# Performance work log

Hardware: AMD Instinct MI355X
Metric: run time of the kernel (lower is better)

Reference implementation:

```python
import jax, jax.numpy as jnp
import numpy as np

N = 100000      # nodes
E = 1600000     # edges (avg degree 16)
D = 64          # in_channels == conv widths == lin width
G = 64          # graphs in batch
OUT = 10        # out_channels


def setup_inputs() -> dict:
    key = jax.random.key(0)
    ks = jax.random.split(key, 20)
    s = 0.1
    inp = {
        "x": jax.random.normal(ks[0], (N, D), jnp.float32),
        "edge_index": jax.random.randint(ks[1], (2, E), 0, N, dtype=jnp.int64),
        "batch": jnp.sort(jax.random.randint(ks[2], (N,), 0, G, dtype=jnp.int64)),
    }
    k = 3
    for i in range(3):  # 3 SAGEConv layers: lin_l (Wl, bl) on aggregated, lin_r (Wr, no bias) on root
        inp[f"c{i}_Wl"] = jax.random.normal(ks[k], (D, D), jnp.float32) * s; k += 1
        inp[f"c{i}_bl"] = jnp.zeros((D,), jnp.float32)
        inp[f"c{i}_Wr"] = jax.random.normal(ks[k], (D, D), jnp.float32) * s; k += 1
    inp["l0_W"] = jax.random.normal(ks[k], (D, D), jnp.float32) * s; k += 1
    inp["l0_b"] = jnp.zeros((D,), jnp.float32)
    inp["out_W"] = jax.random.normal(ks[k], (D, OUT), jnp.float32) * s; k += 1
    inp["out_b"] = jnp.zeros((OUT,), jnp.float32)
    return inp


def reference(x, edge_index, batch,
              c0_Wl, c0_bl, c0_Wr,
              c1_Wl, c1_bl, c1_Wr,
              c2_Wl, c2_bl, c2_Wr,
              l0_W, l0_b, out_W, out_b):
    src, dst = edge_index[0], edge_index[1]
    # in-degree of each target node (mean conv aggregation), computed once
    deg = jax.ops.segment_sum(jnp.ones((E,), x.dtype), dst, num_segments=N)
    inv_deg = (1.0 / jnp.maximum(deg, 1.0))[:, None]

    def sage(h, Wl, bl, Wr):
        # gather source features, mean-aggregate at targets, then lin_l(agg) + lin_r(h)
        agg = jax.ops.segment_sum(h[src], dst, num_segments=N) * inv_deg
        return agg @ Wl + bl + h @ Wr

    h = jax.nn.relu(sage(x, c0_Wl, c0_bl, c0_Wr))
    h = jax.nn.relu(sage(h, c1_Wl, c1_bl, c1_Wr))
    h = jax.nn.relu(sage(h, c2_Wl, c2_bl, c2_Wr))

    # global mean pool over graphs
    cnt = jax.ops.segment_sum(jnp.ones((N,), h.dtype), batch, num_segments=G)
    g = jax.ops.segment_sum(h, batch, num_segments=G) / jnp.maximum(cnt, 1.0)[:, None]

    g = jax.nn.relu(g @ l0_W + l0_b)
    return g @ out_W + out_b  # [G, OUT]
```

## Files before the change

kernel.cpp:

```cpp
#include <hip/hip_runtime.h>
#include <hip/hip_fp16.h>

#define WPB 8
#define PADK 136
#define BSH 8
#define BNODES 256
#define SC_BLOCKS 256
#define HIST_BLOCKS 256
#define HSTRIDE 512

typedef _Float16 half8 __attribute__((ext_vector_type(8)));
typedef _Float16 half2v __attribute__((ext_vector_type(2)));
typedef float floatx4 __attribute__((ext_vector_type(4)));
typedef float floatx2 __attribute__((ext_vector_type(2)));

__global__ __launch_bounds__(256) void gnn_pre(const int* __restrict__ dst,
                                               int* __restrict__ bkt_cnt, int nbkt, int E,
                                               const int* __restrict__ batch,
                                               float* __restrict__ gcnt, int N,
                                               const float4* __restrict__ xin,
                                               ushort4* __restrict__ x16o, int n4,
                                               __half* __restrict__ x16,
                                               __half* __restrict__ hA,
                                               __half* __restrict__ hB,
                                               int* __restrict__ hist_all) {
    int tid = threadIdx.x;
    if (blockIdx.x < HIST_BLOCKS) {
        __shared__ int h[512];
        __shared__ int gb[64];
        for (int i = tid; i < nbkt; i += 256) h[i] = 0;
        if (tid < 64) gb[tid] = 0;
        __syncthreads();
        const int stride = HIST_BLOCKS * 256;
        for (int e = blockIdx.x * 256 + tid; e < E; e += stride)
            atomicAdd(&h[dst[e] >> BSH], 1);
        for (int i = blockIdx.x * 256 + tid; i < N; i += stride)
            atomicAdd(&gb[batch[i]], 1);
        __syncthreads();
        for (int i = tid; i < nbkt; i += 256) {
            int v = h[i];
            hist_all[blockIdx.x * HSTRIDE + i] = v;
            if (v) atomicAdd(&bkt_cnt[i], v);
        }
        if (tid < 64) {
            int v = gb[tid];
            if (v) atomicAdd(&gcnt[tid], (float)v);
        }
        if (blockIdx.x == 0 && tid < 64) {
            x16[(size_t)N * 64 + tid] = __ushort_as_half((unsigned short)0);
            hA[(size_t)N * 64 + tid] = __ushort_as_half((unsigned short)0);
            hB[(size_t)N * 64 + tid] = __ushort_as_half((unsigned short)0);
        }
    } else {
        int i = (blockIdx.x - HIST_BLOCKS) * 256 + tid;
        if (i < n4) {
            float4 f = xin[i];
            ushort4 o;
            o.x = __half_as_ushort(__float2half(f.x));
            o.y = __half_as_ushort(__float2half(f.y));
            o.z = __half_as_ushort(__float2half(f.z));
            o.w = __half_as_ushort(__float2half(f.w));
            x16o[i] = o;
        }
    }
}

__global__ void gnn_bkt_scan(const int* __restrict__ bkt_cnt, int* __restrict__ bkt_base,
                             int* __restrict__ row_ptr, int nbkt, int N) {
    int lane = threadIdx.x;
    int carry = 0;
    for (int base = 0; base < nbkt; base += 64) {
        int idx = base + lane;
        int v = (idx < nbkt) ? bkt_cnt[idx] : 0;
        int x = v;
#pragma unroll
        for (int off = 1; off < 64; off <<= 1) {
            int y = __shfl_up(x, off);
            if (lane >= off) x += y;
        }
        if (idx < nbkt) bkt_base[idx] = carry + (x - v);
        carry += __shfl(x, 63);
    }
    if (lane == 0) {
        bkt_base[nbkt] = carry;
        row_ptr[N] = carry;
    }
}

__global__ __launch_bounds__(256) void gnn_scan2(const int* __restrict__ hist_all,
                                                 const int* __restrict__ bkt_base,
                                                 int* __restrict__ blk_base_all, int nbkt) {
    int b = blockIdx.x;
    int t = threadIdx.x, lane = t & 63, wv = t >> 6;
    __shared__ int wsum[4];
    int v = hist_all[t * HSTRIDE + b];
    int x = v;
#pragma unroll
    for (int off = 1; off < 64; off <<= 1) {
        int y = __shfl_up(x, off);
        if (lane >= off) x += y;
    }
    if (lane == 63) wsum[wv] = x;
    __syncthreads();
    int wexcl = 0;
    for (int w = 0; w < wv; w++) wexcl += wsum[w];
    blk_base_all[t * HSTRIDE + b] = bkt_base[b] + wexcl + (x - v);
}

__global__ __launch_bounds__(256) void gnn_bkt_scatter(const int* __restrict__ src,
                                                       const int* __restrict__ dst,
                                                       const int* __restrict__ blk_base_all,
                                                       unsigned int* __restrict__ pairs,
                                                       int E, int nbkt) {
    __shared__ int cur[512];
    int tid = threadIdx.x;
    for (int i = tid; i < nbkt; i += 256) cur[i] = blk_base_all[blockIdx.x * HSTRIDE + i];
    __syncthreads();
    const int stride = SC_BLOCKS * 256;
    for (int e = blockIdx.x * 256 + tid; e < E; e += stride) {
        int d = dst[e];
        int b = d >> BSH;
        int p = atomicAdd(&cur[b], 1);
        pairs[p] = (unsigned int)src[e] | ((unsigned int)(d & (BNODES - 1)) << 24);
    }
}

__global__ __launch_bounds__(256) void gnn_bkt_csr(const unsigned int* __restrict__ pairs,
                                                   const int* __restrict__ bkt_base,
                                                   int* __restrict__ row_ptr,
                                                   float* __restrict__ inv_deg,
                                                   int* __restrict__ csr_src, int N) {
    __shared__ int hist[BNODES];
    __shared__ int excl[BNODES];
    __shared__ int cur[BNODES];
    int b = blockIdx.x;
    int base = bkt_base[b];
    int cnt = bkt_base[b + 1] - base;
    int nd0 = b << BSH;
    int tid = threadIdx.x;
    hist[tid] = 0;
    __syncthreads();
    for (int i = tid; i < cnt; i += 256) atomicAdd(&hist[pairs[base + i] >> 24], 1);
    __syncthreads();
    if (tid < 64) {
        int carry = 0;
#pragma unroll
        for (int c = 0; c < BNODES; c += 64) {
            int v = hist[c + tid];
            int x = v;
#pragma unroll
            for (int off = 1; off < 64; off <<= 1) {
                int y = __shfl_up(x, off);
                if (tid >= off) x += y;
            }
            excl[c + tid] = carry + (x - v);
            carry += __shfl(x, 63);
        }
    }
    __syncthreads();
    {
        int node = nd0 + tid;
        if (node < N) {
            row_ptr[node] = base + excl[tid];
            int d = hist[tid];
            inv_deg[node] = 1.0f / (float)(d > 1 ? d : 1);
        }
        cur[tid] = excl[tid];
    }
    __syncthreads();
    for (int i = tid; i < cnt; i += 256) {
        unsigned int u = pairs[base + i];
        int j = u >> 24;
        int pos = atomicAdd(&cur[j], 1);
        csr_src[base + pos] = (int)(u & 0xFFFFFFu);
    }
}

#define GATH16(eReg, ibase, accum)                                          \
    {                                                                       \
        floatx2 v[8];                                                       \
        _Pragma("unroll") for (int j = 0; j < 8; j++) {                     \
            int sj = __shfl(eReg, (ibase) + 2 * j + hf);                    \
            half2v hh = hin2v[(size_t)sj * 32 + col];                       \
            floatx2 f;                                                      \
            f.x = (float)hh[0];                                             \
            f.y = (float)hh[1];                                             \
            v[j] = f;                                                       \
        }                                                                   \
        accum += ((v[0] + v[1]) + (v[2] + v[3])) + ((v[4] + v[5]) + (v[6] + v[7])); \
    }

__global__ __launch_bounds__(512, 4) void gnn_sage(const __half* __restrict__ hin,
                                                   __half* __restrict__ hout,
                                                   const int* __restrict__ row_ptr,
                                                   const int* __restrict__ csr_src,
                                                   const float* __restrict__ inv_deg,
                                                   const float* __restrict__ Wl,
                                                   const float* __restrict__ bl,
                                                   const float* __restrict__ Wr, int n) {
    __shared__ _Float16 w_lds[64 * PADK];
    __shared__ _Float16 in_lds[WPB][16 * PADK];
    int tid = threadIdx.x, lane = tid & 63, wv = tid >> 6;
    for (int i = tid; i < 64 * 64; i += 512) {
        int k = i >> 6, nn = i & 63;
        w_lds[nn * PADK + k] = (_Float16)Wl[i];
        w_lds[nn * PADK + 64 + k] = (_Float16)Wr[i];
    }
    __syncthreads();
    int ngroups = (n + 15) >> 4;
    int g = blockIdx.x * WPB + wv;
    if (g >= ngroups) return;
    int m16 = lane & 15, quad = lane >> 4;
    int hf = lane >> 5, col = lane & 31;
    float bias[4];
#pragma unroll
    for (int nt = 0; nt < 4; nt++) bias[nt] = bl[nt * 16 + m16];
    _Float16* my_in = in_lds[wv];
    const unsigned* hin32 = (const unsigned*)hin;
    const half2v* hin2v = (const half2v*)hin;
    int nd0 = g << 4;
    int nclamp = n - 1 - nd0;
    int idx = nd0 + lane;
    int rr = (lane <= 16) ? row_ptr[min(idx, n)] : 0;
    float ig = (lane < 16) ? inv_deg[min(idx, n - 1)] : 0.0f;

#pragma unroll
    for (int jp = 0; jp < 8; jp++) {
        int j2 = jp << 1;
        int nd = nd0 + min(j2 + hf, nclamp);
        unsigned u = hin32[(size_t)nd * 32 + col];
        ((unsigned*)(my_in + (j2 + hf) * PADK + 64))[col] = u;
    }

    int ef[16];
#pragma unroll
    for (int j = 0; j < 16; j++) {
        int jj = min(j, nclamp);
        int s0 = __shfl(rr, jj), s1 = __shfl(rr, jj + 1);
        int cb = min(64, s1 - s0);
        ef[j] = (lane < cb) ? csr_src[s0 + lane] : n;
    }

#pragma unroll
    for (int jp = 0; jp < 8; jp++) {
        int j2 = jp << 1;
        int jjA = min(j2, nclamp), jjB = min(j2 + 1, nclamp);
        int s0A = __shfl(rr, jjA), s1A = __shfl(rr, jjA + 1);
        int s0B = __shfl(rr, jjB), s1B = __shfl(rr, jjB + 1);
        float idgA = __shfl(ig, jjA), idgB = __shfl(ig, jjB);
        int cbA = min(64, s1A - s0A), cbB = min(64, s1B - s0B);
        floatx2 accA, accB;
        accA.x = 0.f; accA.y = 0.f;
        accB.x = 0.f; accB.y = 0.f;
#pragma unroll
        for (int ib = 0; ib < 4; ib++) {
            if (ib * 16 < cbA) GATH16(ef[j2], ib * 16, accA);
            if (ib * 16 < cbB) GATH16(ef[j2 + 1], ib * 16, accB);
        }
        for (int base = s0A + 64; base < s1A; base += 64) {
            int cb = min(64, s1A - base);
            int ei = (lane < cb) ? csr_src[base + lane] : n;
#pragma unroll
            for (int ib = 0; ib < 4; ib++)
                if (ib * 16 < cb) GATH16(ei, ib * 16, accA);
        }
        for (int base = s0B + 64; base < s1B; base += 64) {
            int cb = min(64, s1B - base);
            int ei = (lane < cb) ? csr_src[base + lane] : n;
#pragma unroll
            for (int ib = 0; ib < 4; ib++)
                if (ib * 16 < cb) GATH16(ei, ib * 16, accB);
        }
        accA.x += __shfl_xor(accA.x, 32);
        accA.y += __shfl_xor(accA.y, 32);
        accB.x += __shfl_xor(accB.x, 32);
        accB.y += __shfl_xor(accB.y, 32);
        floatx2 wv2;
        wv2.x = hf ? accB.x * idgB : accA.x * idgA;
        wv2.y = hf ? accB.y * idgB : accA.y * idgA;
        __half2 hw;
        hw.x = __float2half(wv2.x);
        hw.y = __float2half(wv2.y);
        ((__half2*)(my_in + (j2 + hf) * PADK))[col] = hw;
    }
    half8 afrag[4];
    const _Float16* abase = my_in + m16 * PADK + quad * 8;
#pragma unroll
    for (int ks = 0; ks < 4; ks++) afrag[ks] = *(const half8*)(abase + ks * 32);
    floatx4 accv[4];
#pragma unroll
    for (int nt = 0; nt < 4; nt++) {
        accv[nt].x = 0.f; accv[nt].y = 0.f; accv[nt].z = 0.f; accv[nt].w = 0.f;
    }
#pragma unroll
    for (int nt = 0; nt < 4; nt++) {
        const _Float16* bbase = w_lds + (nt * 16 + m16) * PADK + quad * 8;
#pragma unroll
        for (int ks = 0; ks < 4; ks++) {
            half8 bfrag = *(const half8*)(bbase + ks * 32);
            accv[nt] = __builtin_amdgcn_mfma_f32_16x16x32_f16(afrag[ks], bfrag, accv[nt], 0, 0, 0);
        }
    }
#pragma unroll
    for (int nt = 0; nt < 4; nt++) {
#pragma unroll
        for (int r = 0; r < 4; r++) {
            int node = nd0 + quad * 4 + r;
            if (node < n) {
                float v = fmaxf(accv[nt][r] + bias[nt], 0.0f);
                hout[(size_t)node * 64 + nt * 16 + m16] = __float2half(v);
            }
        }
    }
}

__global__ __launch_bounds__(512, 4) void gnn_sage_pool(const __half* __restrict__ hin,
                                                        const int* __restrict__ row_ptr,
                                                        const int* __restrict__ csr_src,
                                                        const float* __restrict__ inv_deg,
                                                        const float* __restrict__ Wl,
                                                        const float* __restrict__ bl,
                                                        const float* __restrict__ Wr,
                                                        const int* __restrict__ batch,
                                                        float* __restrict__ gsum, int n) {
    __shared__ _Float16 w_lds[64 * PADK];
    __shared__ _Float16 in_lds[WPB][16 * PADK];
    int tid = threadIdx.x, lane = tid & 63, wv = tid >> 6;
    for (int i = tid; i < 64 * 64; i += 512) {
        int k = i >> 6, nn = i & 63;
        w_lds[nn * PADK + k] = (_Float16)Wl[i];
        w_lds[nn * PADK + 64 + k] = (_Float16)Wr[i];
    }
    __syncthreads();
    int ngroups = (n + 15) >> 4;
    int g = blockIdx.x * WPB + wv;
    if (g >= ngroups) return;
    int m16 = lane & 15, quad = lane >> 4;
    int hf = lane >> 5, col = lane & 31;
    float bias[4];
#pragma unroll
    for (int nt = 0; nt < 4; nt++) bias[nt] = bl[nt * 16 + m16];
    _Float16* my_in = in_lds[wv];
    const unsigned* hin32 = (const unsigned*)hin;
    const half2v* hin2v = (const half2v*)hin;
    int nd0 = g << 4;
    int nclamp = n - 1 - nd0;
    int idx = nd0 + lane;
    int rr = (lane <= 16) ? row_ptr[min(idx, n)] : 0;
    float ig = (lane < 16) ? inv_deg[min(idx, n - 1)] : 0.0f;

#pragma unroll
    for (int jp = 0; jp < 8; jp++) {
        int j2 = jp << 1;
        int nd = nd0 + min(j2 + hf, nclamp);
        unsigned u = hin32[(size_t)nd * 32 + col];
        ((unsigned*)(my_in + (j2 + hf) * PADK + 64))[col] = u;
    }

    int ef[16];
#pragma unroll
    for (int j = 0; j < 16; j++) {
        int jj = min(j, nclamp);
        int s0 = __shfl(rr, jj), s1 = __shfl(rr, jj + 1);
        int cb = min(64, s1 - s0);
        ef[j] = (lane < cb) ? csr_src[s0 + lane] : n;
    }

#pragma unroll
    for (int jp = 0; jp < 8; jp++) {
        int j2 = jp << 1;
        int jjA = min(j2, nclamp), jjB = min(j2 + 1, nclamp);
        int s0A = __shfl(rr, jjA), s1A = __shfl(rr, jjA + 1);
        int s0B = __shfl(rr, jjB), s1B = __shfl(rr, jjB + 1);
        float idgA = __shfl(ig, jjA), idgB = __shfl(ig, jjB);
        int cbA = min(64, s1A - s0A), cbB = min(64, s1B - s0B);
        floatx2 accA, accB;
        accA.x = 0.f; accA.y = 0.f;
        accB.x = 0.f; accB.y = 0.f;
#pragma unroll
        for (int ib = 0; ib < 4; ib++) {
            if (ib * 16 < cbA) GATH16(ef[j2], ib * 16, accA);
            if (ib * 16 < cbB) GATH16(ef[j2 + 1], ib * 16, accB);
        }
        for (int base = s0A + 64; base < s1A; base += 64) {
            int cb = min(64, s1A - base);
            int ei = (lane < cb) ? csr_src[base + lane] : n;
#pragma unroll
            for (int ib = 0; ib < 4; ib++)
                if (ib * 16 < cb) GATH16(ei, ib * 16, accA);
        }
        for (int base = s0B + 64; base < s1B; base += 64) {
            int cb = min(64, s1B - base);
            int ei = (lane < cb) ? csr_src[base + lane] : n;
#pragma unroll
            for (int ib = 0; ib < 4; ib++)
                if (ib * 16 < cb) GATH16(ei, ib * 16, accB);
        }
        accA.x += __shfl_xor(accA.x, 32);
        accA.y += __shfl_xor(accA.y, 32);
        accB.x += __shfl_xor(accB.x, 32);
        accB.y += __shfl_xor(accB.y, 32);
        floatx2 wv2;
        wv2.x = hf ? accB.x * idgB : accA.x * idgA;
        wv2.y = hf ? accB.y * idgB : accA.y * idgA;
        __half2 hw;
        hw.x = __float2half(wv2.x);
        hw.y = __float2half(wv2.y);
        ((__half2*)(my_in + (j2 + hf) * PADK))[col] = hw;
    }
    half8 afrag[4];
    const _Float16* abase = my_in + m16 * PADK + quad * 8;
#pragma unroll
    for (int ks = 0; ks < 4; ks++) afrag[ks] = *(const half8*)(abase + ks * 32);
    floatx4 accv[4];
#pragma unroll
    for (int nt = 0; nt < 4; nt++) {
        accv[nt].x = 0.f; accv[nt].y = 0.f; accv[nt].z = 0.f; accv[nt].w = 0.f;
    }
#pragma unroll
    for (int nt = 0; nt < 4; nt++) {
        const _Float16* bbase = w_lds + (nt * 16 + m16) * PADK + quad * 8;
#pragma unroll
        for (int ks = 0; ks < 4; ks++) {
            half8 bfrag = *(const half8*)(bbase + ks * 32);
            accv[nt] = __builtin_amdgcn_mfma_f32_16x16x32_f16(afrag[ks], bfrag, accv[nt], 0, 0, 0);
        }
    }
    int bFirst = batch[nd0];
    int bLast = batch[min(nd0 + 15, n - 1)];
    if (bFirst == bLast && nd0 + 15 < n) {
#pragma unroll
        for (int nt = 0; nt < 4; nt++) {
            float s = fmaxf(accv[nt][0] + bias[nt], 0.0f) + fmaxf(accv[nt][1] + bias[nt], 0.0f) +
                      fmaxf(accv[nt][2] + bias[nt], 0.0f) + fmaxf(accv[nt][3] + bias[nt], 0.0f);
            s += __shfl_xor(s, 16);
            s += __shfl_xor(s, 32);
            if (quad == 0) atomicAdd(&gsum[bFirst * 64 + nt * 16 + m16], s);
        }
    } else {
#pragma unroll
        for (int nt = 0; nt < 4; nt++) {
#pragma unroll
            for (int r = 0; r < 4; r++) {
                int node = nd0 + quad * 4 + r;
                if (node < n) {
                    int bg = batch[node];
                    float v = fmaxf(accv[nt][r] + bias[nt], 0.0f);
                    atomicAdd(&gsum[bg * 64 + nt * 16 + m16], v);
                }
            }
        }
    }
}

__global__ __launch_bounds__(256) void gnn_head(const float* __restrict__ gsum,
                                                const float* __restrict__ gcnt,
                                                const float* __restrict__ l0W,
                                                const float* __restrict__ l0b,
                                                const float* __restrict__ outW,
                                                const float* __restrict__ outb,
                                                float* __restrict__ out, int G, int OUT) {
    __shared__ float gm[64 * 64];
    __shared__ float t2[64 * 64];
    int tid = threadIdx.x;
    for (int i = tid; i < G * 64; i += 256) {
        int r = i >> 6;
        gm[i] = gsum[i] / fmaxf(gcnt[r], 1.0f);
    }
    __syncthreads();
    for (int i = tid; i < G * 64; i += 256) {
        int r = i >> 6, c = i & 63;
        float s = l0b[c];
#pragma unroll 8
        for (int k = 0; k < 64; k++) s += gm[(r << 6) + k] * l0W[(k << 6) + c];
        t2[i] = fmaxf(s, 0.0f);
    }
    __syncthreads();
    for (int i = tid; i < G * OUT; i += 256) {
        int r = i / OUT, c = i - r * OUT;
        float s = outb[c];
#pragma unroll 8
        for (int k = 0; k < 64; k++) s += t2[(r << 6) + k] * outW[k * OUT + c];
        out[i] = s;
    }
}

extern "C" void kernel_launch(void* const* d_in, const int* in_sizes, int n_in,
                              void* d_out, int out_size, void* d_ws, size_t ws_size,
                              hipStream_t stream) {
    const float* x = (const float*)d_in[0];
    const int* ei = (const int*)d_in[1];
    const int* batch = (const int*)d_in[2];
    const float* Wl[3] = {(const float*)d_in[3], (const float*)d_in[6], (const float*)d_in[9]};
    const float* bl[3] = {(const float*)d_in[4], (const float*)d_in[7], (const float*)d_in[10]};
    const float* Wr[3] = {(const float*)d_in[5], (const float*)d_in[8], (const float*)d_in[11]};
    const float* l0W = (const float*)d_in[12];
    const float* l0b = (const float*)d_in[13];
    const float* outW = (const float*)d_in[14];
    const float* outb = (const float*)d_in[15];

    int N = in_sizes[2];
    int E = in_sizes[1] / 2;
    int OUT = 10;
    int G = out_size / OUT;
    const int* src = ei;
    const int* dst = ei + E;
    int NBKT = (N + BNODES - 1) >> BSH;

    char* ws = (char*)d_ws;
    size_t off = 0;
    auto alloc = [&](size_t b) -> char* {
        char* p = ws + off;
        off = (off + b + 255) & ~(size_t)255;
        return p;
    };
    int* row_ptr = (int*)alloc((size_t)(N + 1) * 4);
    int* csr_src = (int*)alloc((size_t)E * 4);
    float* inv_deg = (float*)alloc((size_t)N * 4);
    size_t zoff = off;
    int* bkt_cnt = (int*)alloc((size_t)NBKT * 4);
    float* gcnt = (float*)alloc((size_t)G * 4);
    float* gsum = (float*)alloc((size_t)G * 64 * 4);
    size_t zlen = off - zoff;
    int* bkt_base = (int*)alloc((size_t)(NBKT + 1) * 4);
    int* hist_all = (int*)alloc((size_t)HIST_BLOCKS * HSTRIDE * 4);
    int* blk_base_all = (int*)alloc((size_t)HIST_BLOCKS * HSTRIDE * 4);
    unsigned int* pairs = (unsigned int*)alloc((size_t)E * 4);
    __half* x16 = (__half*)alloc((size_t)(N + 1) * 64 * 2);
    __half* hA = (__half*)alloc((size_t)(N + 1) * 64 * 2);
    __half* hB = (__half*)alloc((size_t)(N + 1) * 64 * 2);

    hipMemsetAsync(ws + zoff, 0, zlen, stream);

    int n4 = N * 64 / 4;
    int pre_blocks = HIST_BLOCKS + (n4 + 255) / 256;
    gnn_pre<<<pre_blocks, 256, 0, stream>>>(dst, bkt_cnt, NBKT, E, batch, gcnt, N,
                                            (const float4*)x, (ushort4*)x16, n4,
                                            x16, hA, hB, hist_all);
    gnn_bkt_scan<<<1, 64, 0, stream>>>(bkt_cnt, bkt_base, row_ptr, NBKT, N);
    gnn_scan2<<<NBKT, 256, 0, stream>>>(hist_all, bkt_base, blk_base_all, NBKT);
    gnn_bkt_scatter<<<SC_BLOCKS, 256, 0, stream>>>(src, dst, blk_base_all, pairs, E, NBKT);
    gnn_bkt_csr<<<NBKT, 256, 0, stream>>>(pairs, bkt_base, row_ptr, inv_deg, csr_src, N);

    int ngroups = (N + 15) >> 4;
    int sage_blocks = (ngroups + WPB - 1) / WPB;
    gnn_sage<<<sage_blocks, 512, 0, stream>>>(x16, hA, row_ptr, csr_src, inv_deg,
                                              Wl[0], bl[0], Wr[0], N);
    gnn_sage<<<sage_blocks, 512, 0, stream>>>(hA, hB, row_ptr, csr_src, inv_deg,
                                              Wl[1], bl[1], Wr[1], N);
    gnn_sage_pool<<<sage_blocks, 512, 0, stream>>>(hB, row_ptr, csr_src, inv_deg,
                                                   Wl[2], bl[2], Wr[2], batch, gsum, N);

    gnn_head<<<1, 256, 0, stream>>>(gsum, gcnt, l0W, l0b, outW, outb, (float*)d_out, G, OUT);
}
```

Measured before the change: 324.4 us.

## Gather neighbor rows with 8-byte loads, four edges per wave instruction

The neighbor aggregation now has each wave load 8-byte half4 chunks, with 16 lanes covering one 128-byte row, so four edges are fetched per instruction instead of two with 4-byte loads. The first 16 edges of all 16 nodes are gathered in one unrolled pass up front, which puts many independent loads in flight. Higher-degree nodes then run a second pass that handles the remaining edges. The goal is fewer memory instructions and more latency hiding in this gather-bound kernel. The cost is an extra cross-lane shuffle reduction step, and the 16 float4 accumulators held across the first pass raise register pressure, which could reduce occupancy.

```diff
diff --git a/kernel.cpp b/kernel.cpp
--- a/kernel.cpp
+++ b/kernel.cpp
@@ -10,9 +10,8 @@
 #define HSTRIDE 512
 
 typedef _Float16 half8 __attribute__((ext_vector_type(8)));
-typedef _Float16 half2v __attribute__((ext_vector_type(2)));
+typedef _Float16 half4v __attribute__((ext_vector_type(4)));
 typedef float floatx4 __attribute__((ext_vector_type(4)));
-typedef float floatx2 __attribute__((ext_vector_type(2)));
 
 __global__ __launch_bounds__(256) void gnn_pre(const int* __restrict__ dst,
                                                int* __restrict__ bkt_cnt, int nbkt, int E,
@@ -176,18 +175,14 @@
     }
 }
 
-#define GATH16(eReg, ibase, accum)                                          \
-    {                                                                       \
-        floatx2 v[8];                                                       \
-        _Pragma("unroll") for (int j = 0; j < 8; j++) {                     \
-            int sj = __shfl(eReg, (ibase) + 2 * j + hf);                    \
-            half2v hh = hin2v[(size_t)sj * 32 + col];                       \
-            floatx2 f;                                                      \
-            f.x = (float)hh[0];                                             \
-            f.y = (float)hh[1];                                             \
-            v[j] = f;                                                       \
-        }                                                                   \
-        accum += ((v[0] + v[1]) + (v[2] + v[3])) + ((v[4] + v[5]) + (v[6] + v[7])); \
+#define GATHC(eReg, i0, accum)                                  \
+    {                                                           \
+        int sj_ = __shfl(eReg, (i0) + (lane >> 4));             \
+        half4v h_ = hin4v[(size_t)sj_ * 16 + m16];              \
+        accum.x += (float)h_[0];                                \
+        accum.y += (float)h_[1];                                \
+        accum.z += (float)h_[2];                                \
+        accum.w += (float)h_[3];                                \
     }
 
 __global__ __launch_bounds__(512, 4) void gnn_sage(const __half* __restrict__ hin,
@@ -217,7 +212,7 @@
     for (int nt = 0; nt < 4; nt++) bias[nt] = bl[nt * 16 + m16];
     _Float16* my_in = in_lds[wv];
     const unsigned* hin32 = (const unsigned*)hin;
-    const half2v* hin2v = (const half2v*)hin;
+    const half4v* hin4v = (const half4v*)hin;
     int nd0 = g << 4;
     int nclamp = n - 1 - nd0;
     int idx = nd0 + lane;
@@ -241,48 +236,59 @@
         ef[j] = (lane < cb) ? csr_src[s0 + lane] : n;
     }
 
-#pragma unroll
-    for (int jp = 0; jp < 8; jp++) {
-        int j2 = jp << 1;
-        int jjA = min(j2, nclamp), jjB = min(j2 + 1, nclamp);
-        int s0A = __shfl(rr, jjA), s1A = __shfl(rr, jjA + 1);
-        int s0B = __shfl(rr, jjB), s1B = __shfl(rr, jjB + 1);
-        float idgA = __shfl(ig, jjA), idgB = __shfl(ig, jjB);
-        int cbA = min(64, s1A - s0A), cbB = min(64, s1B - s0B);
-        floatx2 accA, accB;
-        accA.x = 0.f; accA.y = 0.f;
-        accB.x = 0.f; accB.y = 0.f;
-#pragma unroll
-        for (int ib = 0; ib < 4; ib++) {
-            if (ib * 16 < cbA) GATH16(ef[j2], ib * 16, accA);
-            if (ib * 16 < cbB) GATH16(ef[j2 + 1], ib * 16, accB);
-        }
-        for (int base = s0A + 64; base < s1A; base += 64) {
-            int cb = min(64, s1A - base);
-            int ei = (lane < cb) ? csr_src[base + lane] : n;
-#pragma unroll
-            for (int ib = 0; ib < 4; ib++)
-                if (ib * 16 < cb) GATH16(ei, ib * 16, accA);
-        }
-        for (int base = s0B + 64; base < s1B; base += 64) {
-            int cb = min(64, s1B - base);
-            int ei = (lane < cb) ? csr_src[base + lane] : n;
-#pragma unroll
-            for (int ib = 0; ib < 4; ib++)
-                if (ib * 16 < cb) GATH16(ei, ib * 16, accB);
-        }
-        accA.x += __shfl_xor(accA.x, 32);
-        accA.y += __shfl_xor(accA.y, 32);
-        accB.x += __shfl_xor(accB.x, 32);
-        accB.y += __shfl_xor(accB.y, 32);
-        floatx2 wv2;
-        wv2.x = hf ? accB.x * idgB : accA.x * idgA;
-        wv2.y = hf ? accB.y * idgB : accA.y * idgA;
-        __half2 hw;
-        hw.x = __float2half(wv2.x);
-        hw.y = __float2half(wv2.y);
-        ((__half2*)(my_in + (j2 + hf) * PADK))[col] = hw;
-    }
+    floatx4 acc[16];
+#pragma unroll
+    for (int j = 0; j < 16; j++) {
+        floatx4 a = {0.f, 0.f, 0.f, 0.f};
+        GATHC(ef[j], 0, a);
+        GATHC(ef[j], 4, a);
+        GATHC(ef[j], 8, a);
+        GATHC(ef[j], 12, a);
+        acc[j] = a;
+    }
+
+#pragma unroll
+    for (int j = 0; j < 16; j++) {
+        int jj = min(j, nclamp);
+        int s0 = __shfl(rr, jj), s1 = __shfl(rr, jj + 1);
+        int deg = s1 - s0;
+        floatx4 a = acc[j];
+        if (deg > 16) {
+            int dcap = min(deg, 64);
+            for (int c0 = 16; c0 < dcap; c0 += 16) {
+                GATHC(ef[j], c0, a);
+                GATHC(ef[j], c0 + 4, a);
+                GATHC(ef[j], c0 + 8, a);
+                GATHC(ef[j], c0 + 12, a);
+            }
+            for (int base = s0 + 64; base < s1; base += 64) {
+                int cb2 = min(64, s1 - base);
+                int ei = (lane < cb2) ? csr_src[base + lane] : n;
+                for (int i0 = 0; i0 < cb2; i0 += 16) {
+                    GATHC(ei, i0, a);
+                    GATHC(ei, i0 + 4, a);
+                    GATHC(ei, i0 + 8, a);
+                    GATHC(ei, i0 + 12, a);
+                }
+            }
+        }
+        a.x += __shfl_xor(a.x, 16);
+        a.y += __shfl_xor(a.y, 16);
+        a.z += __shfl_xor(a.z, 16);
+        a.w += __shfl_xor(a.w, 16);
+        a.x += __shfl_xor(a.x, 32);
+        a.y += __shfl_xor(a.y, 32);
+        a.z += __shfl_xor(a.z, 32);
+        a.w += __shfl_xor(a.w, 32);
+        float idg = __shfl(ig, jj);
+        half4v hw;
+        hw[0] = (_Float16)(a.x * idg);
+        hw[1] = (_Float16)(a.y * idg);
+        hw[2] = (_Float16)(a.z * idg);
+        hw[3] = (_Float16)(a.w * idg);
+        if (quad == 0) *(half4v*)(my_in + j * PADK + m16 * 4) = hw;
+    }
+
     half8 afrag[4];
     const _Float16* abase = my_in + m16 * PADK + quad * 8;
 #pragma unroll
@@ -342,7 +348,7 @@
     for (int nt = 0; nt < 4; nt++) bias[nt] = bl[nt * 16 + m16];
     _Float16* my_in = in_lds[wv];
     const unsigned* hin32 = (const unsigned*)hin;
-    const half2v* hin2v = (const half2v*)hin;
+    const half4v* hin4v = (const half4v*)hin;
     int nd0 = g << 4;
     int nclamp = n - 1 - nd0;
     int idx = nd0 + lane;
@@ -366,48 +372,59 @@
         ef[j] = (lane < cb) ? csr_src[s0 + lane] : n;
     }
 
-#pragma unroll
-    for (int jp = 0; jp < 8; jp++) {
-        int j2 = jp << 1;
-        int jjA = min(j2, nclamp), jjB = min(j2 + 1, nclamp);
-        int s0A = __shfl(rr, jjA), s1A = __shfl(rr, jjA + 1);
-        int s0B = __shfl(rr, jjB), s1B = __shfl(rr, jjB + 1);
-        float idgA = __shfl(ig, jjA), idgB = __shfl(ig, jjB);
-        int cbA = min(64, s1A - s0A), cbB = min(64, s1B - s0B);
-        floatx2 accA, accB;
-        accA.x = 0.f; accA.y = 0.f;
-        accB.x = 0.f; accB.y = 0.f;
-#pragma unroll
-        for (int ib = 0; ib < 4; ib++) {
-            if (ib * 16 < cbA) GATH16(ef[j2], ib * 16, accA);
-            if (ib * 16 < cbB) GATH16(ef[j2 + 1], ib * 16, accB);
-        }
-        for (int base = s0A + 64; base < s1A; base += 64) {
-            int cb = min(64, s1A - base);
-            int ei = (lane < cb) ? csr_src[base + lane] : n;
-#pragma unroll
-            for (int ib = 0; ib < 4; ib++)
-                if (ib * 16 < cb) GATH16(ei, ib * 16, accA);
-        }
-        for (int base = s0B + 64; base < s1B; base += 64) {
-            int cb = min(64, s1B - base);
-            int ei = (lane < cb) ? csr_src[base + lane] : n;
-#pragma unroll
-            for (int ib = 0; ib < 4; ib++)
-                if (ib * 16 < cb) GATH16(ei, ib * 16, accB);
-        }
-        accA.x += __shfl_xor(accA.x, 32);
-        accA.y += __shfl_xor(accA.y, 32);
-        accB.x += __shfl_xor(accB.x, 32);
-        accB.y += __shfl_xor(accB.y, 32);
-        floatx2 wv2;
-        wv2.x = hf ? accB.x * idgB : accA.x * idgA;
-        wv2.y = hf ? accB.y * idgB : accA.y * idgA;
-        __half2 hw;
-        hw.x = __float2half(wv2.x);
-        hw.y = __float2half(wv2.y);
-        ((__half2*)(my_in + (j2 + hf) * PADK))[col] = hw;
-    }
+    floatx4 acc[16];
+#pragma unroll
+    for (int j = 0; j < 16; j++) {
+        floatx4 a = {0.f, 0.f, 0.f, 0.f};
+        GATHC(ef[j], 0, a);
+        GATHC(ef[j], 4, a);
+        GATHC(ef[j], 8, a);
+        GATHC(ef[j], 12, a);
+        acc[j] = a;
+    }
+
+#pragma unroll
+    for (int j = 0; j < 16; j++) {
+        int jj = min(j, nclamp);
+        int s0 = __shfl(rr, jj), s1 = __shfl(rr, jj + 1);
+        int deg = s1 - s0;
+        floatx4 a = acc[j];
+        if (deg > 16) {
+            int dcap = min(deg, 64);
+            for (int c0 = 16; c0 < dcap; c0 += 16) {
+                GATHC(ef[j], c0, a);
+                GATHC(ef[j], c0 + 4, a);
+                GATHC(ef[j], c0 + 8, a);
+                GATHC(ef[j], c0 + 12, a);
+            }
+            for (int base = s0 + 64; base < s1; base += 64) {
+                int cb2 = min(64, s1 - base);
+                int ei = (lane < cb2) ? csr_src[base + lane] : n;
+                for (int i0 = 0; i0 < cb2; i0 += 16) {
+                    GATHC(ei, i0, a);
+                    GATHC(ei, i0 + 4, a);
+                    GATHC(ei, i0 + 8, a);
+                    GATHC(ei, i0 + 12, a);
+                }
+            }
+        }
+        a.x += __shfl_xor(a.x, 16);
+        a.y += __shfl_xor(a.y, 16);
+        a.z += __shfl_xor(a.z, 16);
+        a.w += __shfl_xor(a.w, 16);
+        a.x += __shfl_xor(a.x, 32);
+        a.y += __shfl_xor(a.y, 32);
+        a.z += __shfl_xor(a.z, 32);
+        a.w += __shfl_xor(a.w, 32);
+        float idg = __shfl(ig, jj);
+        half4v hw;
+        hw[0] = (_Float16)(a.x * idg);
+        hw[1] = (_Float16)(a.y * idg);
+        hw[2] = (_Float16)(a.z * idg);
+        hw[3] = (_Float16)(a.w * idg);
+        if (quad == 0) *(half4v*)(my_in + j * PADK + m16 * 4) = hw;
+    }
+
     half8 afrag[4];
     const _Float16* abase = my_in + m16 * PADK + quad * 8;
 #pragma unroll
```

Result: slower. 487.2 us (+50.2%).
